# Performance work log

Measured on AMD Instinct MI355X. Metric: run time of the kernel, lower is better.

The kernel has to match this reference:

```python
import jax, jax.numpy as jnp
import numpy as np

N_NODES = 50000
N_EDGES = 800000
IN_DIM = 128
HID = 128
N_GRAPHS = 256
N_CLASSES = 2
ALPHA = 0.2  # leaky relu slope
EPS_BN = 1e-5


def setup_inputs() -> dict:
    key = jax.random.key(0)
    ks = jax.random.split(key, 24)
    adjacency = jax.random.randint(ks[0], (2, N_EDGES), 0, N_NODES, dtype=jnp.int32)
    input_feature = jax.random.normal(ks[1], (N_NODES, IN_DIM), dtype=jnp.float32)
    graph_indicator = jnp.sort(jax.random.randint(ks[2], (N_NODES,), 0, N_GRAPHS, dtype=jnp.int32))
    labels = jax.random.randint(ks[3], (N_GRAPHS,), 0, N_CLASSES, dtype=jnp.int64)
    s = 0.05
    params = {
        'W1': jax.random.normal(ks[4], (IN_DIM, HID), jnp.float32) * s,
        'a1': jax.random.normal(ks[5], (2 * HID,), jnp.float32) * s,
        'bn2_g': jnp.ones((HID,), jnp.float32),
        'bn2_b': jnp.zeros((HID,), jnp.float32),
        'W2': jax.random.normal(ks[6], (HID, HID), jnp.float32) * s,
        'a2': jax.random.normal(ks[7], (2 * HID,), jnp.float32) * s,
        'bn3_g': jnp.ones((HID,), jnp.float32),
        'bn3_b': jnp.zeros((HID,), jnp.float32),
        'W3': jax.random.normal(ks[8], (HID, HID), jnp.float32) * s,
        'a3': jax.random.normal(ks[9], (2 * HID,), jnp.float32) * s,
        'fc1_w': jax.random.normal(ks[10], (HID, 2 * HID), jnp.float32) * s,
        'fc1_b': jnp.zeros((2 * HID,), jnp.float32),
        'fc2_w': jax.random.normal(ks[11], (2 * HID, HID), jnp.float32) * s,
        'fc2_b': jnp.zeros((HID,), jnp.float32),
        'fc3_w': jax.random.normal(ks[12], (HID, N_CLASSES), jnp.float32) * s,
        'fc3_b': jnp.zeros((N_CLASSES,), jnp.float32),
    }
    return dict(adjacency=adjacency, input_feature=input_feature,
                graph_indicator=graph_indicator, labels=labels, **params)


def _batchnorm(x, g, b):
    # training-mode BatchNorm1d over node dim (biased variance)
    mu = jnp.mean(x, axis=0)
    var = jnp.mean((x - mu) ** 2, axis=0)
    return (x - mu) * jax.lax.rsqrt(var + EPS_BN) * g + b


def _sp_gat(x, src, dst, W, a):
    # pyGAT SpGraphAttentionLayer (dropout disabled / eval mode)
    h = x @ W                                # [N, F]
    F = h.shape[1]
    e_src = h @ a[:F]                        # [N]
    e_dst = h @ a[F:]                        # [N]
    e = e_src[src] + e_dst[dst]              # [E]
    ee = jnp.exp(-jax.nn.leaky_relu(e, ALPHA))
    rowsum = jax.ops.segment_sum(ee, src, num_segments=N_NODES)          # [N]
    num = jax.ops.segment_sum(ee[:, None] * h[dst], src, num_segments=N_NODES)  # [N, F]
    h_prime = num / (rowsum[:, None] + 1e-16)
    return jax.nn.elu(h_prime)


def reference(adjacency, input_feature, graph_indicator, labels,
              W1, a1, bn2_g, bn2_b, W2, a2, bn3_g, bn3_b, W3, a3,
              fc1_w, fc1_b, fc2_w, fc2_b, fc3_w, fc3_b):
    src, dst = adjacency[0], adjacency[1]
    # bn1 output is discarded in the original forward
    x = _sp_gat(input_feature, src, dst, W1, a1)
    x = _batchnorm(x, bn2_g, bn2_b)
    x = _sp_gat(x, src, dst, W2, a2)
    x = _batchnorm(x, bn3_g, bn3_b)
    x = _sp_gat(x, src, dst, W3, a3)
    # pooling_sum_4tensor: per-graph sum pooling
    pooled = jax.ops.segment_sum(x, graph_indicator, num_segments=N_GRAPHS)  # [G, F]
    x = jax.nn.relu(pooled @ fc1_w + fc1_b)
    x = jax.nn.relu(x @ fc2_w + fc2_b)
    logits = x @ fc3_w + fc3_b
    return logits
```

## Files before the change

### kernel.cpp

```cpp
#include <hip/hip_runtime.h>
#include <hip/hip_bf16.h>

#define N_NODES 50000
#define N_EDGES 800000
#define FD 128
#define N_GRAPHS 256
#define NPART 6250

typedef unsigned short u16;
typedef short bf16x8 __attribute__((ext_vector_type(8)));
typedef float f32x4 __attribute__((ext_vector_type(4)));

__device__ __forceinline__ u16 f2bf(float v) {
    __hip_bfloat16 h = __float2bfloat16(v);
    union { __hip_bfloat16 hh; u16 u; } c; c.hh = h; return c.u;
}
__device__ __forceinline__ float bf2f(u16 r) {
    return __uint_as_float(((unsigned int)r) << 16);
}

__global__ __launch_bounds__(256) void count_deg_part_k(const int* __restrict__ src,
                                                        int* __restrict__ cnt, int E) {
    int part = blockIdx.x & 7;
    int lo = part * NPART, hi = lo + NPART;
    int stride = (gridDim.x >> 3) * 256;
    for (int e = (blockIdx.x >> 3) * 256 + threadIdx.x; e < E; e += stride) {
        int s = src[e];
        if (s >= lo && s < hi) atomicAdd(&cnt[s], 1);
    }
}

__global__ __launch_bounds__(256) void fill_csr_part_k(const int* __restrict__ src,
                                                       const int* __restrict__ dst,
                                                       int* __restrict__ cur,
                                                       int* __restrict__ edst, int E) {
    int part = blockIdx.x & 7;
    int lo = part * NPART, hi = lo + NPART;
    int stride = (gridDim.x >> 3) * 256;
    for (int e = (blockIdx.x >> 3) * 256 + threadIdx.x; e < E; e += stride) {
        int s = src[e];
        if (s >= lo && s < hi) {
            int p = atomicAdd(&cur[s], 1);
            edst[p] = dst[e];
        }
    }
}

__global__ __launch_bounds__(256) void scan1_k(const int* __restrict__ cnt,
                                               int* __restrict__ bsum, int M) {
    int i = blockIdx.x * 256 + threadIdx.x;
    int v = (i < M) ? cnt[i] : 0;
    __shared__ int l[256];
    l[threadIdx.x] = v;
    __syncthreads();
    for (int s = 128; s > 0; s >>= 1) {
        if (threadIdx.x < s) l[threadIdx.x] += l[threadIdx.x + s];
        __syncthreads();
    }
    if (threadIdx.x == 0) bsum[blockIdx.x] = l[0];
}

__global__ __launch_bounds__(256) void scan2_k(int* __restrict__ bsum, int NB,
                                               float* __restrict__ z) {
    int tid = threadIdx.x;
    z[tid] = 0.f; z[tid + 256] = 0.f;
    int v = (tid < NB) ? bsum[tid] : 0;
    __shared__ int l[256];
    l[tid] = v;
    __syncthreads();
    for (int off = 1; off < 256; off <<= 1) {
        int t = (tid >= off) ? l[tid - off] : 0;
        __syncthreads();
        l[tid] += t;
        __syncthreads();
    }
    if (tid < NB) bsum[tid] = l[tid] - v;
}

__global__ __launch_bounds__(256) void scan3_k(const int* __restrict__ cnt,
                                               const int* __restrict__ bsum,
                                               int* __restrict__ offs,
                                               int* __restrict__ cur, int M) {
    int i = blockIdx.x * 256 + threadIdx.x;
    int tid = threadIdx.x;
    int v = (i < M) ? cnt[i] : 0;
    __shared__ int l[256];
    l[tid] = v;
    __syncthreads();
    for (int off = 1; off < 256; off <<= 1) {
        int t = (tid >= off) ? l[tid - off] : 0;
        __syncthreads();
        l[tid] += t;
        __syncthreads();
    }
    int excl = l[tid] - v + bsum[blockIdx.x];
    if (i < M) { offs[i] = excl; cur[i] = excl; }
    if (i == M - 1) offs[M] = excl + v;
}

__global__ __launch_bounds__(128) void wprep1_k(const float* __restrict__ W,
                                                u16* __restrict__ Wt,
                                                float* __restrict__ cvec) {
    int n = blockIdx.x, k = threadIdx.x;
    Wt[(size_t)n * FD + k] = f2bf(W[(size_t)k * FD + n]);
    if (k == 0) cvec[n] = 0.f;
}

__global__ __launch_bounds__(128) void bnfw_k(const float* __restrict__ W,
                                              const float* __restrict__ sums,
                                              const float* __restrict__ sumsq,
                                              const float* __restrict__ g,
                                              const float* __restrict__ b,
                                              float invN,
                                              u16* __restrict__ Wt,
                                              float* __restrict__ cvec) {
    int n = blockIdx.x, k = threadIdx.x;
    __shared__ float scs[128], shs[128], l[128];
    float mu = sums[k] * invN;
    float var = sumsq[k] * invN - mu * mu;
    float sc = g[k] * rsqrtf(var + 1e-5f);
    scs[k] = sc;
    shs[k] = b[k] - mu * sc;
    __syncthreads();
    float w = W[(size_t)k * FD + n];
    Wt[(size_t)n * FD + k] = f2bf(scs[k] * w);
    l[k] = shs[k] * w;
    __syncthreads();
    for (int s = 64; s > 0; s >>= 1) {
        if (k < s) l[k] += l[k + s];
        __syncthreads();
    }
    if (k == 0) cvec[n] = l[0];
}

__global__ __launch_bounds__(256) void gemm_mfma_k(const float* __restrict__ Xf,
                                                   const u16* __restrict__ Xb,
                                                   int use_f32,
                                                   const u16* __restrict__ Wt,
                                                   const float* __restrict__ cvec,
                                                   const float* __restrict__ avec,
                                                   u16* __restrict__ Hb,
                                                   float* __restrict__ es,
                                                   float* __restrict__ ed, int M) {
    __shared__ u16 As[64][136];
    __shared__ u16 Bs[128][136];
    __shared__ float sa_s[128], sa_d[128], cv[128];
    int tid = threadIdx.x;
    if (tid < 128) { sa_s[tid] = avec[tid]; sa_d[tid] = avec[128 + tid]; cv[tid] = cvec[tid]; }
    int row0 = blockIdx.x * 64;
    {
        int n = tid >> 1, k0 = (tid & 1) * 64;
        const uint4* s = (const uint4*)(Wt + (size_t)n * FD + k0);
#pragma unroll
        for (int u = 0; u < 8; u++) *(uint4*)&Bs[n][k0 + u * 8] = s[u];
    }
    {
        int r = tid >> 2, k0 = (tid & 3) * 32;
        int grow = row0 + r;
        if (grow < M) {
            if (use_f32) {
                const float4* s = (const float4*)(Xf + (size_t)grow * FD + k0);
#pragma unroll
                for (int u = 0; u < 8; u++) {
                    float4 v = s[u];
                    ushort4 o;
                    o.x = f2bf(v.x); o.y = f2bf(v.y); o.z = f2bf(v.z); o.w = f2bf(v.w);
                    *(ushort4*)&As[r][k0 + u * 4] = o;
                }
            } else {
                const uint4* s = (const uint4*)(Xb + (size_t)grow * FD + k0);
#pragma unroll
                for (int u = 0; u < 4; u++) *(uint4*)&As[r][k0 + u * 8] = s[u];
            }
        } else {
            uint4 z = make_uint4(0, 0, 0, 0);
#pragma unroll
            for (int u = 0; u < 4; u++) *(uint4*)&As[r][k0 + u * 8] = z;
        }
    }
    __syncthreads();

    int wave = tid >> 6, lane = tid & 63;
    int quad = lane >> 4, n16 = lane & 15;
    int rbase = wave * 16;
    f32x4 acc[8];
    f32x4 zz = {0.f, 0.f, 0.f, 0.f};
#pragma unroll
    for (int t = 0; t < 8; t++) acc[t] = zz;

#pragma unroll
    for (int kk = 0; kk < 128; kk += 32) {
        bf16x8 a = *(const bf16x8*)&As[rbase + n16][kk + quad * 8];
#pragma unroll
        for (int t = 0; t < 8; t++) {
            bf16x8 b = *(const bf16x8*)&Bs[t * 16 + n16][kk + quad * 8];
            acc[t] = __builtin_amdgcn_mfma_f32_16x16x32_bf16(a, b, acc[t], 0, 0, 0);
        }
    }

#pragma unroll
    for (int reg = 0; reg < 4; reg++) {
        int grow = row0 + rbase + quad * 4 + reg;
        float vals[8];
        float ps = 0.f, pd = 0.f;
#pragma unroll
        for (int t = 0; t < 8; t++) {
            float v = acc[t][reg] + cv[t * 16 + n16];
            vals[t] = v;
            ps += v * sa_s[t * 16 + n16];
            pd += v * sa_d[t * 16 + n16];
        }
#pragma unroll
        for (int o = 8; o > 0; o >>= 1) { ps += __shfl_xor(ps, o); pd += __shfl_xor(pd, o); }
        if (grow < M) {
            if (n16 == 0) { es[grow] = ps; ed[grow] = pd; }
#pragma unroll
            for (int t = 0; t < 8; t++)
                Hb[(size_t)grow * FD + t * 16 + n16] = f2bf(vals[t]);
        }
    }
}

__global__ __launch_bounds__(256) void agg_k(const u16* __restrict__ Hb,
                                             const float* __restrict__ es_,
                                             const float* __restrict__ ed_,
                                             const int* __restrict__ offs,
                                             const int* __restrict__ edst,
                                             u16* __restrict__ Out, int M) {
    int node = __builtin_amdgcn_readfirstlane((int)((blockIdx.x * blockDim.x + threadIdx.x) >> 6));
    int lane = threadIdx.x & 63;
    if (node >= M) return;
    int s0 = offs[node], s1 = offs[node + 1];
    float esv = es_[node];
    const unsigned int* Hrow = (const unsigned int*)Hb;
    float2 a0 = make_float2(0.f, 0.f), a1 = make_float2(0.f, 0.f);
    float2 a2 = make_float2(0.f, 0.f), a3 = make_float2(0.f, 0.f);
    float rs = 0.f;
    int e = s0;
    for (; e + 8 <= s1; e += 8) {
        int d[8];
#pragma unroll
        for (int u = 0; u < 8; u++) d[u] = __builtin_amdgcn_readfirstlane(edst[e + u]);
        float w[8];
#pragma unroll
        for (int u = 0; u < 8; u++) {
            float ev = esv + ed_[d[u]];
            float lr = ev > 0.f ? ev : 0.2f * ev;
            w[u] = __expf(-lr);
        }
        unsigned int r[8];
#pragma unroll
        for (int u = 0; u < 8; u++) r[u] = Hrow[(size_t)d[u] * 64 + lane];
#pragma unroll
        for (int u = 0; u < 8; u++) {
            rs += w[u];
            float2* ac = (u & 3) == 0 ? &a0 : (u & 3) == 1 ? &a1 : (u & 3) == 2 ? &a2 : &a3;
            ac->x += w[u] * __int_as_float(r[u] << 16);
            ac->y += w[u] * __int_as_float(r[u] & 0xffff0000u);
        }
    }
    for (; e < s1; e++) {
        int d = __builtin_amdgcn_readfirstlane(edst[e]);
        float ev = esv + ed_[d];
        float lr = ev > 0.f ? ev : 0.2f * ev;
        float wv = __expf(-lr);
        rs += wv;
        unsigned int r = Hrow[(size_t)d * 64 + lane];
        a0.x += wv * __int_as_float(r << 16);
        a0.y += wv * __int_as_float(r & 0xffff0000u);
    }
    float inv = 1.f / (rs + 1e-16f);
    float vx = (a0.x + a1.x + a2.x + a3.x) * inv;
    float vy = (a0.y + a1.y + a2.y + a3.y) * inv;
    vx = vx > 0.f ? vx : (__expf(vx) - 1.f);
    vy = vy > 0.f ? vy : (__expf(vy) - 1.f);
    unsigned int pk = ((unsigned int)f2bf(vy) << 16) | f2bf(vx);
    ((unsigned int*)Out)[(size_t)node * 64 + lane] = pk;
}

__global__ void bnstats_b_k(const u16* __restrict__ Xb, float* __restrict__ sums,
                            float* __restrict__ sumsq, int M) {
    int f = threadIdx.x & 127;
    int half = threadIdx.x >> 7;
    float s1 = 0.f, s2 = 0.f;
    for (int r = blockIdx.x * 2 + half; r < M; r += gridDim.x * 2) {
        float v = bf2f(Xb[(size_t)r * FD + f]);
        s1 += v; s2 += v * v;
    }
    __shared__ float l1[256], l2[256];
    l1[threadIdx.x] = s1; l2[threadIdx.x] = s2;
    __syncthreads();
    if (half == 0) {
        atomicAdd(&sums[f], l1[f] + l1[f + 128]);
        atomicAdd(&sumsq[f], l2[f] + l2[f + 128]);
    }
}

__global__ void pool_k(const u16* __restrict__ Xb, const int* __restrict__ gi,
                       float* __restrict__ pooled, int M) {
    int f = threadIdx.x & 127;
    int half = threadIdx.x >> 7;
    int r0 = blockIdx.x * 128 + half;
    int rend = min(blockIdx.x * 128 + 128, M);
    int curg = -1; float acc = 0.f;
    for (int r = r0; r < rend; r += 2) {
        int g = gi[r];
        if (g != curg) {
            if (curg >= 0) atomicAdd(&pooled[(size_t)curg * FD + f], acc);
            curg = g; acc = 0.f;
        }
        acc += bf2f(Xb[(size_t)r * FD + f]);
    }
    if (curg >= 0) atomicAdd(&pooled[(size_t)curg * FD + f], acc);
}

__global__ __launch_bounds__(256) void mlp_k(const float* __restrict__ pooled,
                                             const float* __restrict__ fc1w, const float* __restrict__ fc1b,
                                             const float* __restrict__ fc2w, const float* __restrict__ fc2b,
                                             const float* __restrict__ fc3w, const float* __restrict__ fc3b,
                                             float* __restrict__ out) {
    int g = blockIdx.x, j = threadIdx.x;
    __shared__ float x[128], t1[256], t2[128], p0[128], p1[128];
    if (j < 128) x[j] = pooled[(size_t)g * FD + j];
    __syncthreads();
    float s = fc1b[j];
    for (int k = 0; k < 128; k++) s += x[k] * fc1w[(size_t)k * 256 + j];
    t1[j] = fmaxf(s, 0.f);
    __syncthreads();
    if (j < 128) {
        float s2 = fc2b[j];
        for (int k = 0; k < 256; k++) s2 += t1[k] * fc2w[(size_t)k * 128 + j];
        t2[j] = fmaxf(s2, 0.f);
    }
    __syncthreads();
    if (j < 128) { p0[j] = t2[j] * fc3w[j * 2]; p1[j] = t2[j] * fc3w[j * 2 + 1]; }
    __syncthreads();
    for (int s3 = 64; s3 > 0; s3 >>= 1) {
        if (j < s3) { p0[j] += p0[j + s3]; p1[j] += p1[j + s3]; }
        __syncthreads();
    }
    if (j == 0) { out[g * 2] = p0[0] + fc3b[0]; out[g * 2 + 1] = p1[0] + fc3b[1]; }
}

extern "C" void kernel_launch(void* const* d_in, const int* in_sizes, int n_in,
                              void* d_out, int out_size, void* d_ws, size_t ws_size,
                              hipStream_t stream) {
    const int*   adj  = (const int*)d_in[0];
    const float* xin  = (const float*)d_in[1];
    const int*   gi   = (const int*)d_in[2];
    const float* W1   = (const float*)d_in[4];
    const float* a1   = (const float*)d_in[5];
    const float* bn2g = (const float*)d_in[6];
    const float* bn2b = (const float*)d_in[7];
    const float* W2   = (const float*)d_in[8];
    const float* a2   = (const float*)d_in[9];
    const float* bn3g = (const float*)d_in[10];
    const float* bn3b = (const float*)d_in[11];
    const float* W3   = (const float*)d_in[12];
    const float* a3   = (const float*)d_in[13];
    const float* fc1w = (const float*)d_in[14];
    const float* fc1b = (const float*)d_in[15];
    const float* fc2w = (const float*)d_in[16];
    const float* fc2b = (const float*)d_in[17];
    const float* fc3w = (const float*)d_in[18];
    const float* fc3b = (const float*)d_in[19];
    float* out = (float*)d_out;

    const int N = N_NODES, E = N_EDGES, G = N_GRAPHS;

    u16*   Xb     = (u16*)d_ws;
    u16*   Hb     = Xb + (size_t)N * FD;
    u16*   Wt     = Hb + (size_t)N * FD;
    float* es     = (float*)(Wt + FD * FD);
    float* ed     = es + N;
    float* bnbuf  = ed + N;
    float* sumsA  = bnbuf;
    float* sumsqA = bnbuf + 128;
    float* sumsB  = bnbuf + 256;
    float* sumsqB = bnbuf + 384;
    float* cvec   = bnbuf + 512;
    float* pooled = cvec + FD;
    int*   degcnt = (int*)(pooled + (size_t)G * FD);
    int*   offs   = degcnt + N;
    int*   cur    = offs + (N + 2);
    int*   bsum   = cur + N;
    int*   edst   = bsum + 256;

    const int* srcp = adj;
    const int* dstp = adj + E;

    const int NB = (N + 255) / 256;

    hipMemsetAsync(degcnt, 0, (size_t)N * sizeof(int), stream);
    count_deg_part_k<<<8 * 392, 256, 0, stream>>>(srcp, degcnt, E);
    scan1_k<<<NB, 256, 0, stream>>>(degcnt, bsum, N);
    scan2_k<<<1, 256, 0, stream>>>(bsum, NB, bnbuf);
    scan3_k<<<NB, 256, 0, stream>>>(degcnt, bsum, offs, cur, N);
    fill_csr_part_k<<<8 * 392, 256, 0, stream>>>(srcp, dstp, cur, edst, E);

    const int gemm_grid = (N + 63) / 64;
    const int wave_grid = (N + 3) / 4;
    const float invN = 1.0f / (float)N;

    wprep1_k<<<FD, 128, 0, stream>>>(W1, Wt, cvec);
    gemm_mfma_k<<<gemm_grid, 256, 0, stream>>>(xin, Xb, 1, Wt, cvec, a1, Hb, es, ed, N);
    agg_k<<<wave_grid, 256, 0, stream>>>(Hb, es, ed, offs, edst, Xb, N);
    bnstats_b_k<<<256, 256, 0, stream>>>(Xb, sumsA, sumsqA, N);

    bnfw_k<<<FD, 128, 0, stream>>>(W2, sumsA, sumsqA, bn2g, bn2b, invN, Wt, cvec);
    gemm_mfma_k<<<gemm_grid, 256, 0, stream>>>(nullptr, Xb, 0, Wt, cvec, a2, Hb, es, ed, N);
    agg_k<<<wave_grid, 256, 0, stream>>>(Hb, es, ed, offs, edst, Xb, N);
    bnstats_b_k<<<256, 256, 0, stream>>>(Xb, sumsB, sumsqB, N);

    bnfw_k<<<FD, 128, 0, stream>>>(W3, sumsB, sumsqB, bn3g, bn3b, invN, Wt, cvec);
    gemm_mfma_k<<<gemm_grid, 256, 0, stream>>>(nullptr, Xb, 0, Wt, cvec, a3, Hb, es, ed, N);
    agg_k<<<wave_grid, 256, 0, stream>>>(Hb, es, ed, offs, edst, Xb, N);

    hipMemsetAsync(pooled, 0, (size_t)G * FD * sizeof(float), stream);
    pool_k<<<(N + 127) / 128, 256, 0, stream>>>(Xb, gi, pooled, N);
    mlp_k<<<G, 256, 0, stream>>>(pooled, fc1w, fc1b, fc2w, fc2b, fc3w, fc3b, out);
}
```

Baseline: 432.6 us.

## Fuse BN stats into aggregation and merge scan stages to cut launches

Batch-norm sum and sum-of-squares are now accumulated inside the aggregation kernel through a per-block shared-memory reduction and atomics into eight partitioned slots. This removes the separate stats pass that re-read the full node feature matrix. The single-block scan2 kernel is folded into scan3, where every block redundantly scans the block sums, and the zeroing of the BN buffers and pooled output moves into scan1, dropping a memset. The cost is a __syncthreads and global atomics in every aggregation block, plus redundant per-block scan work.

```diff
diff --git a/kernel.cpp b/kernel.cpp
--- a/kernel.cpp
+++ b/kernel.cpp
@@ -47,7 +47,9 @@
 }
 
 __global__ __launch_bounds__(256) void scan1_k(const int* __restrict__ cnt,
-                                               int* __restrict__ bsum, int M) {
+                                               int* __restrict__ bsum, int M,
+                                               float* __restrict__ bnbuf,
+                                               float* __restrict__ pooled) {
     int i = blockIdx.x * 256 + threadIdx.x;
     int v = (i < M) ? cnt[i] : 0;
     __shared__ int l[256];
@@ -58,31 +60,28 @@
         __syncthreads();
     }
     if (threadIdx.x == 0) bsum[blockIdx.x] = l[0];
-}
-
-__global__ __launch_bounds__(256) void scan2_k(int* __restrict__ bsum, int NB,
-                                               float* __restrict__ z) {
-    int tid = threadIdx.x;
-    z[tid] = 0.f; z[tid + 256] = 0.f;
-    int v = (tid < NB) ? bsum[tid] : 0;
-    __shared__ int l[256];
-    l[tid] = v;
-    __syncthreads();
-    for (int off = 1; off < 256; off <<= 1) {
-        int t = (tid >= off) ? l[tid - off] : 0;
-        __syncthreads();
-        l[tid] += t;
-        __syncthreads();
-    }
-    if (tid < NB) bsum[tid] = l[tid] - v;
+    if (blockIdx.x == 0) {
+        for (int k = threadIdx.x; k < 4096; k += 256) bnbuf[k] = 0.f;
+        for (int k = threadIdx.x; k < N_GRAPHS * FD; k += 256) pooled[k] = 0.f;
+    }
 }
 
 __global__ __launch_bounds__(256) void scan3_k(const int* __restrict__ cnt,
                                                const int* __restrict__ bsum,
                                                int* __restrict__ offs,
-                                               int* __restrict__ cur, int M) {
+                                               int* __restrict__ cur, int M, int NB) {
     int i = blockIdx.x * 256 + threadIdx.x;
     int tid = threadIdx.x;
+    __shared__ int bs[256];
+    bs[tid] = (tid < NB) ? bsum[tid] : 0;
+    __syncthreads();
+    for (int off = 1; off < 256; off <<= 1) {
+        int t = (tid >= off) ? bs[tid - off] : 0;
+        __syncthreads();
+        bs[tid] += t;
+        __syncthreads();
+    }
+    int base = (blockIdx.x == 0) ? 0 : bs[blockIdx.x - 1];
     int v = (i < M) ? cnt[i] : 0;
     __shared__ int l[256];
     l[tid] = v;
@@ -93,7 +92,7 @@
         l[tid] += t;
         __syncthreads();
     }
-    int excl = l[tid] - v + bsum[blockIdx.x];
+    int excl = l[tid] - v + base;
     if (i < M) { offs[i] = excl; cur[i] = excl; }
     if (i == M - 1) offs[M] = excl + v;
 }
@@ -107,8 +106,8 @@
 }
 
 __global__ __launch_bounds__(128) void bnfw_k(const float* __restrict__ W,
-                                              const float* __restrict__ sums,
-                                              const float* __restrict__ sumsq,
+                                              const float* __restrict__ sums8,
+                                              const float* __restrict__ sumsq8,
                                               const float* __restrict__ g,
                                               const float* __restrict__ b,
                                               float invN,
@@ -116,8 +115,11 @@
                                               float* __restrict__ cvec) {
     int n = blockIdx.x, k = threadIdx.x;
     __shared__ float scs[128], shs[128], l[128];
-    float mu = sums[k] * invN;
-    float var = sumsq[k] * invN - mu * mu;
+    float s = 0.f, q = 0.f;
+#pragma unroll
+    for (int p = 0; p < 8; p++) { s += sums8[p * 128 + k]; q += sumsq8[p * 128 + k]; }
+    float mu = s * invN;
+    float var = q * invN - mu * mu;
     float sc = g[k] * rsqrtf(var + 1e-5f);
     scs[k] = sc;
     shs[k] = b[k] - mu * sc;
@@ -126,8 +128,8 @@
     Wt[(size_t)n * FD + k] = f2bf(scs[k] * w);
     l[k] = shs[k] * w;
     __syncthreads();
-    for (int s = 64; s > 0; s >>= 1) {
-        if (k < s) l[k] += l[k + s];
+    for (int st = 64; st > 0; st >>= 1) {
+        if (k < st) l[k] += l[k + st];
         __syncthreads();
     }
     if (k == 0) cvec[n] = l[0];
@@ -226,73 +228,79 @@
                                              const float* __restrict__ ed_,
                                              const int* __restrict__ offs,
                                              const int* __restrict__ edst,
-                                             u16* __restrict__ Out, int M) {
-    int node = __builtin_amdgcn_readfirstlane((int)((blockIdx.x * blockDim.x + threadIdx.x) >> 6));
-    int lane = threadIdx.x & 63;
-    if (node >= M) return;
-    int s0 = offs[node], s1 = offs[node + 1];
-    float esv = es_[node];
-    const unsigned int* Hrow = (const unsigned int*)Hb;
-    float2 a0 = make_float2(0.f, 0.f), a1 = make_float2(0.f, 0.f);
-    float2 a2 = make_float2(0.f, 0.f), a3 = make_float2(0.f, 0.f);
-    float rs = 0.f;
-    int e = s0;
-    for (; e + 8 <= s1; e += 8) {
-        int d[8];
-#pragma unroll
-        for (int u = 0; u < 8; u++) d[u] = __builtin_amdgcn_readfirstlane(edst[e + u]);
-        float w[8];
-#pragma unroll
-        for (int u = 0; u < 8; u++) {
-            float ev = esv + ed_[d[u]];
+                                             u16* __restrict__ Out,
+                                             float* __restrict__ sums8,
+                                             float* __restrict__ sumsq8,
+                                             int do_bn, int M) {
+    int tid = threadIdx.x;
+    int wavein = tid >> 6;
+    int node = __builtin_amdgcn_readfirstlane((int)(blockIdx.x * 4 + wavein));
+    int lane = tid & 63;
+    __shared__ float4 red[4][64];
+    float vx = 0.f, vy = 0.f;
+    if (node < M) {
+        int s0 = offs[node], s1 = offs[node + 1];
+        float esv = es_[node];
+        const unsigned int* Hrow = (const unsigned int*)Hb;
+        float2 a0 = make_float2(0.f, 0.f), a1 = make_float2(0.f, 0.f);
+        float2 a2 = make_float2(0.f, 0.f), a3 = make_float2(0.f, 0.f);
+        float rs = 0.f;
+        int e = s0;
+        for (; e + 8 <= s1; e += 8) {
+            int d[8];
+#pragma unroll
+            for (int u = 0; u < 8; u++) d[u] = __builtin_amdgcn_readfirstlane(edst[e + u]);
+            float w[8];
+#pragma unroll
+            for (int u = 0; u < 8; u++) {
+                float ev = esv + ed_[d[u]];
+                float lr = ev > 0.f ? ev : 0.2f * ev;
+                w[u] = __expf(-lr);
+            }
+            unsigned int r[8];
+#pragma unroll
+            for (int u = 0; u < 8; u++) r[u] = Hrow[(size_t)d[u] * 64 + lane];
+#pragma unroll
+            for (int u = 0; u < 8; u++) {
+                rs += w[u];
+                float2* ac = (u & 3) == 0 ? &a0 : (u & 3) == 1 ? &a1 : (u & 3) == 2 ? &a2 : &a3;
+                ac->x += w[u] * __int_as_float(r[u] << 16);
+                ac->y += w[u] * __int_as_float(r[u] & 0xffff0000u);
+            }
+        }
+        for (; e < s1; e++) {
+            int d = __builtin_amdgcn_readfirstlane(edst[e]);
+            float ev = esv + ed_[d];
             float lr = ev > 0.f ? ev : 0.2f * ev;
-            w[u] = __expf(-lr);
-        }
-        unsigned int r[8];
-#pragma unroll
-        for (int u = 0; u < 8; u++) r[u] = Hrow[(size_t)d[u] * 64 + lane];
-#pragma unroll
-        for (int u = 0; u < 8; u++) {
-            rs += w[u];
-            float2* ac = (u & 3) == 0 ? &a0 : (u & 3) == 1 ? &a1 : (u & 3) == 2 ? &a2 : &a3;
-            ac->x += w[u] * __int_as_float(r[u] << 16);
-            ac->y += w[u] * __int_as_float(r[u] & 0xffff0000u);
-        }
-    }
-    for (; e < s1; e++) {
-        int d = __builtin_amdgcn_readfirstlane(edst[e]);
-        float ev = esv + ed_[d];
-        float lr = ev > 0.f ? ev : 0.2f * ev;
-        float wv = __expf(-lr);
-        rs += wv;
-        unsigned int r = Hrow[(size_t)d * 64 + lane];
-        a0.x += wv * __int_as_float(r << 16);
-        a0.y += wv * __int_as_float(r & 0xffff0000u);
-    }
-    float inv = 1.f / (rs + 1e-16f);
-    float vx = (a0.x + a1.x + a2.x + a3.x) * inv;
-    float vy = (a0.y + a1.y + a2.y + a3.y) * inv;
-    vx = vx > 0.f ? vx : (__expf(vx) - 1.f);
-    vy = vy > 0.f ? vy : (__expf(vy) - 1.f);
-    unsigned int pk = ((unsigned int)f2bf(vy) << 16) | f2bf(vx);
-    ((unsigned int*)Out)[(size_t)node * 64 + lane] = pk;
-}
-
-__global__ void bnstats_b_k(const u16* __restrict__ Xb, float* __restrict__ sums,
-                            float* __restrict__ sumsq, int M) {
-    int f = threadIdx.x & 127;
-    int half = threadIdx.x >> 7;
-    float s1 = 0.f, s2 = 0.f;
-    for (int r = blockIdx.x * 2 + half; r < M; r += gridDim.x * 2) {
-        float v = bf2f(Xb[(size_t)r * FD + f]);
-        s1 += v; s2 += v * v;
-    }
-    __shared__ float l1[256], l2[256];
-    l1[threadIdx.x] = s1; l2[threadIdx.x] = s2;
-    __syncthreads();
-    if (half == 0) {
-        atomicAdd(&sums[f], l1[f] + l1[f + 128]);
-        atomicAdd(&sumsq[f], l2[f] + l2[f + 128]);
+            float wv = __expf(-lr);
+            rs += wv;
+            unsigned int r = Hrow[(size_t)d * 64 + lane];
+            a0.x += wv * __int_as_float(r << 16);
+            a0.y += wv * __int_as_float(r & 0xffff0000u);
+        }
+        float inv = 1.f / (rs + 1e-16f);
+        vx = (a0.x + a1.x + a2.x + a3.x) * inv;
+        vy = (a0.y + a1.y + a2.y + a3.y) * inv;
+        vx = vx > 0.f ? vx : (__expf(vx) - 1.f);
+        vy = vy > 0.f ? vy : (__expf(vy) - 1.f);
+        unsigned int pk = ((unsigned int)f2bf(vy) << 16) | f2bf(vx);
+        ((unsigned int*)Out)[(size_t)node * 64 + lane] = pk;
+    }
+    if (do_bn) {
+        red[wavein][lane] = make_float4(vx, vy, vx * vx, vy * vy);
+        __syncthreads();
+        if (tid < 64) {
+            float4 a = red[0][tid], b = red[1][tid], c = red[2][tid], d = red[3][tid];
+            float sx = a.x + b.x + c.x + d.x;
+            float sy = a.y + b.y + c.y + d.y;
+            float qx = a.z + b.z + c.z + d.z;
+            float qy = a.w + b.w + c.w + d.w;
+            int part = (int)(blockIdx.x & 7);
+            atomicAdd(&sums8[part * 128 + 2 * tid], sx);
+            atomicAdd(&sums8[part * 128 + 2 * tid + 1], sy);
+            atomicAdd(&sumsq8[part * 128 + 2 * tid], qx);
+            atomicAdd(&sumsq8[part * 128 + 2 * tid + 1], qy);
+        }
     }
 }
 
@@ -374,11 +382,11 @@
     float* es     = (float*)(Wt + FD * FD);
     float* ed     = es + N;
     float* bnbuf  = ed + N;
-    float* sumsA  = bnbuf;
-    float* sumsqA = bnbuf + 128;
-    float* sumsB  = bnbuf + 256;
-    float* sumsqB = bnbuf + 384;
-    float* cvec   = bnbuf + 512;
+    float* sums8A  = bnbuf;
+    float* sumsq8A = bnbuf + 1024;
+    float* sums8B  = bnbuf + 2048;
+    float* sumsq8B = bnbuf + 3072;
+    float* cvec   = bnbuf + 4096;
     float* pooled = cvec + FD;
     int*   degcnt = (int*)(pooled + (size_t)G * FD);
     int*   offs   = degcnt + N;
@@ -393,9 +401,8 @@
 
     hipMemsetAsync(degcnt, 0, (size_t)N * sizeof(int), stream);
     count_deg_part_k<<<8 * 392, 256, 0, stream>>>(srcp, degcnt, E);
-    scan1_k<<<NB, 256, 0, stream>>>(degcnt, bsum, N);
-    scan2_k<<<1, 256, 0, stream>>>(bsum, NB, bnbuf);
-    scan3_k<<<NB, 256, 0, stream>>>(degcnt, bsum, offs, cur, N);
+    scan1_k<<<NB, 256, 0, stream>>>(degcnt, bsum, N, bnbuf, pooled);
+    scan3_k<<<NB, 256, 0, stream>>>(degcnt, bsum, offs, cur, N, NB);
     fill_csr_part_k<<<8 * 392, 256, 0, stream>>>(srcp, dstp, cur, edst, E);
 
     const int gemm_grid = (N + 63) / 64;
@@ -404,19 +411,16 @@
 
     wprep1_k<<<FD, 128, 0, stream>>>(W1, Wt, cvec);
     gemm_mfma_k<<<gemm_grid, 256, 0, stream>>>(xin, Xb, 1, Wt, cvec, a1, Hb, es, ed, N);
-    agg_k<<<wave_grid, 256, 0, stream>>>(Hb, es, ed, offs, edst, Xb, N);
-    bnstats_b_k<<<256, 256, 0, stream>>>(Xb, sumsA, sumsqA, N);
-
-    bnfw_k<<<FD, 128, 0, stream>>>(W2, sumsA, sumsqA, bn2g, bn2b, invN, Wt, cvec);
+    agg_k<<<wave_grid, 256, 0, stream>>>(Hb, es, ed, offs, edst, Xb, sums8A, sumsq8A, 1, N);
+
+    bnfw_k<<<FD, 128, 0, stream>>>(W2, sums8A, sumsq8A, bn2g, bn2b, invN, Wt, cvec);
     gemm_mfma_k<<<gemm_grid, 256, 0, stream>>>(nullptr, Xb, 0, Wt, cvec, a2, Hb, es, ed, N);
-    agg_k<<<wave_grid, 256, 0, stream>>>(Hb, es, ed, offs, edst, Xb, N);
-    bnstats_b_k<<<256, 256, 0, stream>>>(Xb, sumsB, sumsqB, N);
-
-    bnfw_k<<<FD, 128, 0, stream>>>(W3, sumsB, sumsqB, bn3g, bn3b, invN, Wt, cvec);
+    agg_k<<<wave_grid, 256, 0, stream>>>(Hb, es, ed, offs, edst, Xb, sums8B, sumsq8B, 1, N);
+
+    bnfw_k<<<FD, 128, 0, stream>>>(W3, sums8B, sumsq8B, bn3g, bn3b, invN, Wt, cvec);
     gemm_mfma_k<<<gemm_grid, 256, 0, stream>>>(nullptr, Xb, 0, Wt, cvec, a3, Hb, es, ed, N);
-    agg_k<<<wave_grid, 256, 0, stream>>>(Hb, es, ed, offs, edst, Xb, N);
-
-    hipMemsetAsync(pooled, 0, (size_t)G * FD * sizeof(float), stream);
+    agg_k<<<wave_grid, 256, 0, stream>>>(Hb, es, ed, offs, edst, Xb, nullptr, nullptr, 0, N);
+
     pool_k<<<(N + 127) / 128, 256, 0, stream>>>(Xb, gi, pooled, N);
     mlp_k<<<G, 256, 0, stream>>>(pooled, fc1w, fc1b, fc2w, fc2b, fc3w, fc3b, out);
 }
```

New measurement: 477.2 us. 1.1x slower.
